# Optimization experiments

Measured on AMD Instinct MI355X. Metric: run time of the kernel, lower is better.

## Reference

```python
import jax, jax.numpy as jnp
import numpy as np

N_VARS, N_FACT, N_EDGES, D = 100000, 50000, 1000000, 128


def setup_inputs() -> dict:
    key = jax.random.key(0)
    ks = jax.random.split(key, 8)
    variables = jax.random.normal(ks[0], (N_VARS, D), dtype=jnp.float32)
    factors = jax.random.normal(ks[1], (N_FACT, D), dtype=jnp.float32)
    v_to_f = jax.random.randint(ks[2], (N_EDGES,), 0, N_VARS, dtype=jnp.int32)
    f_to_v = jax.random.randint(ks[3], (N_EDGES,), 0, N_FACT, dtype=jnp.int32)
    edge_attr = jax.random.normal(ks[4], (N_EDGES,), dtype=jnp.float32)
    # small init scale to keep activations sane
    W_msg = jax.random.normal(ks[5], (2 * D + 1, D), dtype=jnp.float32) * 0.05
    b_msg = jnp.zeros((D,), dtype=jnp.float32)
    W_comb = jax.random.normal(ks[6], (2 * D, D), dtype=jnp.float32) * 0.05
    b_comb = jnp.zeros((D,), dtype=jnp.float32)
    return dict(variables=variables, factors=factors, v_to_f=v_to_f,
                f_to_v=f_to_v, edge_attr=edge_attr, W_msg=W_msg, b_msg=b_msg,
                W_comb=W_comb, b_comb=b_comb)


def reference(variables, factors, v_to_f, f_to_v, edge_attr, W_msg, b_msg, W_comb, b_comb):
    # gather endpoint features per edge
    x_i = variables[v_to_f]                      # [E, D]
    x_j = factors[f_to_v]                        # [E, D]
    ea = jnp.zeros_like(edge_attr)[:, None]      # forward passes zeros_like(edge_attr)
    # per-edge message MLP (Linear + activation)
    m = jax.nn.relu(jnp.concatenate([x_i, x_j, ea], axis=-1) @ W_msg + b_msg)  # [E, D]
    # scatter-aggregate messages onto the variable (sender) nodes
    aggr_m = jax.ops.segment_sum(m, v_to_f, num_segments=variables.shape[0])   # [N_v, D]
    # concat + combine MLP + residual
    h = jax.nn.relu(jnp.concatenate([variables, aggr_m], axis=-1) @ W_comb + b_comb)
    return variables + h
```

## Files before the change

### kernel.cpp

```cpp
#include <hip/hip_runtime.h>

#define NV 100000
#define NF 50000
#define NE 1000000
#define NBV2 782
#define NBF2 391
#define NBH2 489

typedef unsigned short ushort_t;
typedef unsigned int uint_t;
typedef __attribute__((ext_vector_type(8))) short bf16x8;
typedef __attribute__((ext_vector_type(8))) _Float16 f16x8;
typedef __attribute__((ext_vector_type(2))) _Float16 f16x2;
typedef __attribute__((ext_vector_type(4))) float f32x4;
typedef __attribute__((ext_vector_type(4))) uint_t u32x4;


__device__ inline ushort_t f2bf(float x) {
    union { float f; uint_t u; } c; c.f = x;
    uint_t r = c.u + 0x7fffu + ((c.u >> 16) & 1u);
    return (ushort_t)(r >> 16);
}

__device__ inline uint_t packh2(float a, float b) {
    auto h = __builtin_amdgcn_cvt_pkrtz(a, b);
    return __builtin_bit_cast(uint_t, h);
}

__device__ inline bf16x8 cvt_frag(float4 lo, float4 hi) {
    uint_t a, b, c, d;
    asm("v_cvt_pk_bf16_f32 %0, %1, %2" : "=v"(a) : "v"(lo.x), "v"(lo.y));
    asm("v_cvt_pk_bf16_f32 %0, %1, %2" : "=v"(b) : "v"(lo.z), "v"(lo.w));
    asm("v_cvt_pk_bf16_f32 %0, %1, %2" : "=v"(c) : "v"(hi.x), "v"(hi.y));
    asm("v_cvt_pk_bf16_f32 %0, %1, %2" : "=v"(d) : "v"(hi.z), "v"(hi.w));
    u32x4 q = {a, b, c, d};
    return __builtin_bit_cast(bf16x8, q);
}

__device__ inline void gload_lds16(const void* g, void* l) {
    __builtin_amdgcn_global_load_lds(
        (const __attribute__((address_space(1))) void*)g,
        (__attribute__((address_space(3))) void*)l, 16, 0, 0);
}

__global__ __launch_bounds__(256) void scan_reduce(const int* __restrict__ deg, int* __restrict__ bsum) {
    __shared__ int s[256];
    int t = threadIdx.x, b = blockIdx.x;
    int base = b * 1024 + t * 4;
    int acc = 0;
#pragma unroll
    for (int j = 0; j < 4; j++) { int i = base + j; if (i < NV) acc += deg[i]; }
    s[t] = acc; __syncthreads();
    for (int off = 128; off > 0; off >>= 1) {
        if (t < off) s[t] += s[t + off];
        __syncthreads();
    }
    if (t == 0) bsum[b] = s[0];
}

__global__ __launch_bounds__(128) void scan_mid(int* __restrict__ bsum, int* __restrict__ offs, int nblk) {
    __shared__ int s[128];
    int t = threadIdx.x;
    int val = (t < nblk) ? bsum[t] : 0;
    s[t] = val; __syncthreads();
    for (int off = 1; off < 128; off <<= 1) {
        int x = (t >= off) ? s[t - off] : 0;
        __syncthreads();
        s[t] += x;
        __syncthreads();
    }
    if (t < nblk) bsum[t] = s[t] - val;
    if (t == 0) offs[NV] = NE;
}

__global__ __launch_bounds__(256) void scan_final(int* __restrict__ deg, const int* __restrict__ bsum,
                                                  int* __restrict__ offs) {
    __shared__ int s[256];
    int t = threadIdx.x, b = blockIdx.x;
    int base = b * 1024 + t * 4;
    int v[4];
#pragma unroll
    for (int j = 0; j < 4; j++) { int i = base + j; v[j] = (i < NV) ? deg[i] : 0; }
    int l = v[0] + v[1] + v[2] + v[3];
    s[t] = l; __syncthreads();
    for (int off = 1; off < 256; off <<= 1) {
        int x = (t >= off) ? s[t - off] : 0;
        __syncthreads();
        s[t] += x;
        __syncthreads();
    }
    int run = bsum[b] + s[t] - l;
#pragma unroll
    for (int j = 0; j < 4; j++) {
        int i = base + j;
        if (i < NV) { offs[i] = run; deg[i] = run; }
        run += v[j];
    }
}

__global__ __launch_bounds__(256) void scatter_k(const int* __restrict__ vtf, const int* __restrict__ ftv,
                                                 int* __restrict__ cursor, ushort_t* __restrict__ sf) {
    int e2 = blockIdx.x * 256 + threadIdx.x;
    if (e2 < NE / 2) {
        int2 v = *(const int2*)(vtf + e2 * 2);
        int2 f = *(const int2*)(ftv + e2 * 2);
        int p0 = atomicAdd(&cursor[v.x], 1);
        sf[p0] = (ushort_t)f.x;
        int p1 = atomicAdd(&cursor[v.y], 1);
        sf[p1] = (ushort_t)f.y;
    }
}

__global__ __launch_bounds__(256) void prep_w(const float* __restrict__ Wm, const float* __restrict__ Wc,
                                              ushort_t* __restrict__ frag) {
    int t = blockIdx.x * 256 + threadIdx.x;
    int mat = t >> 14;
    int idx = t & 16383;
    int k = idx >> 7, n = idx & 127;
    int srck = k;
    if (mat == 3) {
        int j = k >> 1;
        srck = (j & 15) + 32 * (j >> 4) + 16 * (k & 1);
    }
    const float* src = (mat < 2) ? (Wm + (size_t)mat * 16384) : (Wc + (size_t)(mat - 2) * 16384);
    float v = src[(size_t)srck * 128 + n];
    ushort_t outv;
    if (mat == 3) {
        _Float16 h = (_Float16)v;
        outv = __builtin_bit_cast(ushort_t, h);
    } else {
        outv = f2bf(v);
    }
    int kc = k >> 5, kk = k & 31, quad = kk >> 3, j = kk & 7;
    int ct = n >> 4, np = n & 15, lane = np + 16 * quad;
    frag[(size_t)mat * 16384 + (size_t)((kc * 8 + ct) * 64 + lane) * 8 + j] = outv;
}

__global__ __launch_bounds__(512, 4) void gemm_msg(const float* __restrict__ V,
                                                   const float* __restrict__ F,
                                                   const ushort_t* __restrict__ wfm,
                                                   const float* __restrict__ bias,
                                                   uint_t* __restrict__ u,
                                                   uint_t* __restrict__ w,
                                                   const int* __restrict__ vtf,
                                                   int* __restrict__ deg) {
    if (blockIdx.x < NBH2) {
        int e4 = blockIdx.x * 512 + threadIdx.x;
        if (e4 < NE / 4) {
            int4 vv = *(const int4*)(vtf + (size_t)e4 * 4);
            atomicAdd(&deg[vv.x], 1);
            atomicAdd(&deg[vv.y], 1);
            atomicAdd(&deg[vv.z], 1);
            atomicAdd(&deg[vv.w], 1);
        }
        return;
    }
    __shared__ ushort_t Bs[16384];

    const int bid = blockIdx.x - NBH2;
    const float* A; const ushort_t* wf; uint_t* C; const float* bs; int M, r0;
    if (bid < NBV2) { A = V; wf = wfm;         C = u; bs = bias;    M = NV; r0 = bid * 128; }
    else            { A = F; wf = wfm + 16384; C = w; bs = nullptr; M = NF; r0 = (bid - NBV2) * 128; }

    const int wv = threadIdx.x >> 6;
    const int lane = threadIdx.x & 63;
    const int quad = lane >> 4, np = lane & 15;
    const int arow = r0 + wv * 16 + np;
    const int ar = (arow < M) ? arow : (M - 1);

    {
        const char* gsrc = (const char*)wf;
        char* lbase = (char*)Bs;
#pragma unroll
        for (int i = 0; i < 4; i++) {
            int off = (wv * 4 + i) * 1024;
            gload_lds16(gsrc + off + lane * 16, lbase + off);
        }
    }
    const float* ap = A + (size_t)ar * 128 + quad * 8;
    float4 vlo[4], vhi[4];
#pragma unroll
    for (int kc = 0; kc < 4; kc++) {
        vlo[kc] = *(const float4*)(ap + kc * 32);
        vhi[kc] = *(const float4*)(ap + kc * 32 + 4);
    }
    float bb0[4], bb1[4];
#pragma unroll
    for (int g = 0; g < 4; g++) {
        bb0[g] = bs ? bs[np + 32 * g] : 0.f;
        bb1[g] = bs ? bs[np + 32 * g + 16] : 0.f;
    }

    __builtin_amdgcn_sched_barrier(0);
    asm volatile("s_waitcnt vmcnt(0)");
    __syncthreads();

    bf16x8 a[4];
#pragma unroll
    for (int kc = 0; kc < 4; kc++) a[kc] = cvt_frag(vlo[kc], vhi[kc]);

    f32x4 acc[8];
#pragma unroll
    for (int ct = 0; ct < 8; ct++) acc[ct] = (f32x4){0.f, 0.f, 0.f, 0.f};

#pragma unroll
    for (int kc = 0; kc < 4; kc++) {
        const ushort_t* wp = Bs + (size_t)(kc * 8 * 64 + lane) * 8;
#pragma unroll
        for (int ct = 0; ct < 8; ct++) {
            bf16x8 b = *(const bf16x8*)(wp + ct * 512);
            acc[ct] = __builtin_amdgcn_mfma_f32_16x16x32_bf16(a[kc], b, acc[ct], 0, 0, 0);
        }
    }

#pragma unroll
    for (int g = 0; g < 4; g++) {
#pragma unroll
        for (int r = 0; r < 4; r++) {
            int orow = r0 + wv * 16 + quad * 4 + r;
            if (orow < M)
                C[(size_t)orow * 64 + g * 16 + np] = packh2(acc[2 * g][r] + bb0[g],
                                                            acc[2 * g + 1][r] + bb1[g]);
        }
    }
}

__global__ __launch_bounds__(256, 6) void aggregate(const uint_t* __restrict__ u32,
                                                    const uint_t* __restrict__ w32,
                                                    const int* __restrict__ offs,
                                                    const ushort_t* __restrict__ sf,
                                                    uint_t* __restrict__ aggr32) {
    int v = (blockIdx.x * 256 + threadIdx.x) >> 6;
    int lane = threadIdx.x & 63;
    if (v >= NV) return;
    int i0 = offs[v], i1 = offs[v + 1];
    f16x2 uh = __builtin_bit_cast(f16x2, u32[(size_t)v * 64 + lane]);
    const f16x2 z2 = __builtin_bit_cast(f16x2, 0u);
    f16x2 acc[8];
#pragma unroll
    for (int j = 0; j < 8; j++) acc[j] = z2;
    for (int i = i0; i < i1; i += 8) {
        int f[8];
#pragma unroll
        for (int j = 0; j < 8; j++) {
            int idx = i + j; if (idx > i1 - 1) idx = i1 - 1;
            f[j] = sf[idx];
        }
        uint_t p[8];
#pragma unroll
        for (int j = 0; j < 8; j++) p[j] = w32[(size_t)f[j] * 64 + lane];
#pragma unroll
        for (int j = 0; j < 8; j++) {
            uint_t pj = (i + j < i1) ? p[j] : 0xFC00FC00u;
            f16x2 s = uh + __builtin_bit_cast(f16x2, pj);
            f16x2 r;
            asm("v_pk_max_f16 %0, %1, %2" : "=v"(r) : "v"(s), "v"(z2));
            acc[j] += r;
        }
    }
    f16x2 t0 = (acc[0] + acc[1]) + (acc[2] + acc[3]);
    f16x2 t1 = (acc[4] + acc[5]) + (acc[6] + acc[7]);
    f16x2 tt = t0 + t1;
    aggr32[(size_t)v * 64 + lane] = __builtin_bit_cast(uint_t, tt);
}

__global__ __launch_bounds__(512, 4) void gemm_final(const float* __restrict__ V,
                                                     const ushort_t* __restrict__ aggr,
                                                     const ushort_t* __restrict__ wfc,
                                                     const float* __restrict__ bias,
                                                     float* __restrict__ OUT, int M) {
    __shared__ ushort_t Bs[32768];

    const int wv = threadIdx.x >> 6;
    const int lane = threadIdx.x & 63;
    const int quad = lane >> 4, np = lane & 15;
    const int r0 = blockIdx.x * 128;
    const int arow = r0 + wv * 16 + np;
    const int ar = (arow < M) ? arow : (M - 1);

    {
        const char* gsrc = (const char*)wfc;
        char* lbase = (char*)Bs;
#pragma unroll
        for (int i = 0; i < 8; i++) {
            int off = (wv * 8 + i) * 1024;
            gload_lds16(gsrc + off + lane * 16, lbase + off);
        }
    }
    const float* ap = V + (size_t)ar * 128 + quad * 8;
    float4 vlo[4], vhi[4];
#pragma unroll
    for (int kc = 0; kc < 4; kc++) {
        vlo[kc] = *(const float4*)(ap + kc * 32);
        vhi[kc] = *(const float4*)(ap + kc * 32 + 4);
    }
    const ushort_t* agp = aggr + (size_t)ar * 128 + quad * 8;
    f16x8 af[4];
#pragma unroll
    for (int kc = 0; kc < 4; kc++) af[kc] = *(const f16x8*)(agp + kc * 32);
    float bb[8];
#pragma unroll
    for (int ct = 0; ct < 8; ct++) bb[ct] = bias[ct * 16 + np];

    __builtin_amdgcn_sched_barrier(0);
    asm volatile("s_waitcnt vmcnt(0)");
    __syncthreads();

    bf16x8 abf[4];
#pragma unroll
    for (int kc = 0; kc < 4; kc++) abf[kc] = cvt_frag(vlo[kc], vhi[kc]);

    f32x4 acc[8];
#pragma unroll
    for (int ct = 0; ct < 8; ct++) acc[ct] = (f32x4){0.f, 0.f, 0.f, 0.f};

#pragma unroll
    for (int kc = 0; kc < 4; kc++) {
        const ushort_t* wp = Bs + (size_t)(kc * 8 * 64 + lane) * 8;
#pragma unroll
        for (int ct = 0; ct < 8; ct++) {
            bf16x8 b = *(const bf16x8*)(wp + ct * 512);
            acc[ct] = __builtin_amdgcn_mfma_f32_16x16x32_bf16(abf[kc], b, acc[ct], 0, 0, 0);
        }
    }
#pragma unroll
    for (int kc = 0; kc < 4; kc++) {
        const ushort_t* wp = Bs + 16384 + (size_t)(kc * 8 * 64 + lane) * 8;
#pragma unroll
        for (int ct = 0; ct < 8; ct++) {
            f16x8 b = *(const f16x8*)(wp + ct * 512);
            acc[ct] = __builtin_amdgcn_mfma_f32_16x16x32_f16(af[kc], b, acc[ct], 0, 0, 0);
        }
    }

    const int orow0 = r0 + wv * 16 + quad * 4;
    float resid[32];
#pragma unroll
    for (int ct = 0; ct < 8; ct++)
#pragma unroll
        for (int r = 0; r < 4; r++) {
            int orow = orow0 + r;
            resid[ct * 4 + r] = (orow < M) ? V[(size_t)orow * 128 + ct * 16 + np] : 0.f;
        }
#pragma unroll
    for (int ct = 0; ct < 8; ct++)
#pragma unroll
        for (int r = 0; r < 4; r++) {
            int orow = orow0 + r;
            if (orow < M)
                OUT[(size_t)orow * 128 + ct * 16 + np] =
                    resid[ct * 4 + r] + fmaxf(acc[ct][r] + bb[ct], 0.f);
        }
}

extern "C" void kernel_launch(void* const* d_in, const int* in_sizes, int n_in,
                              void* d_out, int out_size, void* d_ws, size_t ws_size,
                              hipStream_t stream) {
    const float* variables = (const float*)d_in[0];
    const float* factors   = (const float*)d_in[1];
    const int*   v_to_f    = (const int*)d_in[2];
    const int*   f_to_v    = (const int*)d_in[3];
    const float* W_msg     = (const float*)d_in[5];
    const float* b_msg     = (const float*)d_in[6];
    const float* W_comb    = (const float*)d_in[7];
    const float* b_comb    = (const float*)d_in[8];
    float* out = (float*)d_out;

    ushort_t* wfrag = (ushort_t*)d_ws;
    uint_t*   u     = (uint_t*)(wfrag + 4 * 16384);
    uint_t*   w     = u + (size_t)NV * 64;
    uint_t*   aggr  = w + (size_t)NF * 64;
    ushort_t* sf    = (ushort_t*)(aggr + (size_t)NV * 64);
    int*      deg   = (int*)(sf + NE);
    int*      offs  = deg + NV;
    int*      bsum  = offs + NV + 1;

    const int NBLK = (NV + 1023) / 1024;

    prep_w<<<256, 256, 0, stream>>>(W_msg, W_comb, wfrag);

    hipMemsetAsync(deg, 0, (size_t)NV * sizeof(int), stream);

    gemm_msg<<<NBH2 + NBV2 + NBF2, 512, 0, stream>>>(variables, factors, wfrag, b_msg,
                                                     u, w, v_to_f, deg);

    scan_reduce<<<NBLK, 256, 0, stream>>>(deg, bsum);
    scan_mid<<<1, 128, 0, stream>>>(bsum, offs, NBLK);
    scan_final<<<NBLK, 256, 0, stream>>>(deg, bsum, offs);
    scatter_k<<<(NE / 2 + 255) / 256, 256, 0, stream>>>(v_to_f, f_to_v, deg, sf);

    aggregate<<<(NV * 64) / 256, 256, 0, stream>>>(u, w, offs, sf, aggr);

    gemm_final<<<NBV2, 512, 0, stream>>>(variables, (const ushort_t*)aggr, wfrag + 2 * 16384,
                                         b_comb, out, NV);
}
```

Measured before the change: 317.7 us.

## Process multiple row tiles per GEMM block with prefetch and split histogram kernel

Both GEMM kernels now cover 256 rows per block, looping over sub-tiles. Each block loads the weight fragment into LDS once and reuses it, and prefetches the next tile's activations into registers while the current tile's MFMAs run. gemm_msg drops to 256 threads per block. The degree histogram moves from extra blocks of gemm_msg into its own kernel launch. This amortizes the weight staging per block and hides the global load latency, at the cost of fewer blocks (less parallelism) and an extra launch.

```diff
diff --git a/kernel.cpp b/kernel.cpp
--- a/kernel.cpp
+++ b/kernel.cpp
@@ -3,9 +3,9 @@
 #define NV 100000
 #define NF 50000
 #define NE 1000000
-#define NBV2 782
-#define NBF2 391
-#define NBH2 489
+#define GMV 391
+#define GMF 196
+#define GFN 391
 
 typedef unsigned short ushort_t;
 typedef unsigned int uint_t;
@@ -41,6 +41,17 @@
     __builtin_amdgcn_global_load_lds(
         (const __attribute__((address_space(1))) void*)g,
         (__attribute__((address_space(3))) void*)l, 16, 0, 0);
+}
+
+__global__ __launch_bounds__(256) void hist_k(const int* __restrict__ vtf, int* __restrict__ deg) {
+    int e4 = blockIdx.x * 256 + threadIdx.x;
+    if (e4 < NE / 4) {
+        int4 v = *(const int4*)(vtf + (size_t)e4 * 4);
+        atomicAdd(&deg[v.x], 1);
+        atomicAdd(&deg[v.y], 1);
+        atomicAdd(&deg[v.z], 1);
+        atomicAdd(&deg[v.w], 1);
+    }
 }
 
 __global__ __launch_bounds__(256) void scan_reduce(const int* __restrict__ deg, int* __restrict__ bsum) {
@@ -136,53 +147,39 @@
     frag[(size_t)mat * 16384 + (size_t)((kc * 8 + ct) * 64 + lane) * 8 + j] = outv;
 }
 
-__global__ __launch_bounds__(512, 4) void gemm_msg(const float* __restrict__ V,
+__global__ __launch_bounds__(256, 4) void gemm_msg(const float* __restrict__ V,
                                                    const float* __restrict__ F,
                                                    const ushort_t* __restrict__ wfm,
                                                    const float* __restrict__ bias,
                                                    uint_t* __restrict__ u,
-                                                   uint_t* __restrict__ w,
-                                                   const int* __restrict__ vtf,
-                                                   int* __restrict__ deg) {
-    if (blockIdx.x < NBH2) {
-        int e4 = blockIdx.x * 512 + threadIdx.x;
-        if (e4 < NE / 4) {
-            int4 vv = *(const int4*)(vtf + (size_t)e4 * 4);
-            atomicAdd(&deg[vv.x], 1);
-            atomicAdd(&deg[vv.y], 1);
-            atomicAdd(&deg[vv.z], 1);
-            atomicAdd(&deg[vv.w], 1);
-        }
-        return;
-    }
+                                                   uint_t* __restrict__ w) {
     __shared__ ushort_t Bs[16384];
 
-    const int bid = blockIdx.x - NBH2;
     const float* A; const ushort_t* wf; uint_t* C; const float* bs; int M, r0;
-    if (bid < NBV2) { A = V; wf = wfm;         C = u; bs = bias;    M = NV; r0 = bid * 128; }
-    else            { A = F; wf = wfm + 16384; C = w; bs = nullptr; M = NF; r0 = (bid - NBV2) * 128; }
+    if (blockIdx.x < GMV) { A = V; wf = wfm;         C = u; bs = bias;    M = NV; r0 = blockIdx.x * 256; }
+    else                  { A = F; wf = wfm + 16384; C = w; bs = nullptr; M = NF; r0 = (blockIdx.x - GMV) * 256; }
 
     const int wv = threadIdx.x >> 6;
     const int lane = threadIdx.x & 63;
     const int quad = lane >> 4, np = lane & 15;
-    const int arow = r0 + wv * 16 + np;
-    const int ar = (arow < M) ? arow : (M - 1);
 
     {
         const char* gsrc = (const char*)wf;
         char* lbase = (char*)Bs;
-#pragma unroll
-        for (int i = 0; i < 4; i++) {
-            int off = (wv * 4 + i) * 1024;
-            gload_lds16(gsrc + off + lane * 16, lbase + off);
-        }
-    }
-    const float* ap = A + (size_t)ar * 128 + quad * 8;
+        int toff = threadIdx.x * 16;
+#pragma unroll
+        for (int i = 0; i < 8; i++) gload_lds16(gsrc + i * 4096 + toff, lbase + i * 4096 + toff);
+    }
+
     float4 vlo[4], vhi[4];
-#pragma unroll
-    for (int kc = 0; kc < 4; kc++) {
-        vlo[kc] = *(const float4*)(ap + kc * 32);
-        vhi[kc] = *(const float4*)(ap + kc * 32 + 4);
+    {
+        int ar0 = r0 + wv * 16 + np; if (ar0 >= M) ar0 = M - 1;
+        const float* ap = A + (size_t)ar0 * 128 + quad * 8;
+#pragma unroll
+        for (int kc = 0; kc < 4; kc++) {
+            vlo[kc] = *(const float4*)(ap + kc * 32);
+            vhi[kc] = *(const float4*)(ap + kc * 32 + 4);
+        }
     }
     float bb0[4], bb1[4];
 #pragma unroll
@@ -191,36 +188,49 @@
         bb1[g] = bs ? bs[np + 32 * g + 16] : 0.f;
     }
 
+    asm volatile("s_waitcnt vmcnt(0)" ::: "memory");
     __builtin_amdgcn_sched_barrier(0);
-    asm volatile("s_waitcnt vmcnt(0)");
     __syncthreads();
 
-    bf16x8 a[4];
-#pragma unroll
-    for (int kc = 0; kc < 4; kc++) a[kc] = cvt_frag(vlo[kc], vhi[kc]);
-
-    f32x4 acc[8];
-#pragma unroll
-    for (int ct = 0; ct < 8; ct++) acc[ct] = (f32x4){0.f, 0.f, 0.f, 0.f};
-
-#pragma unroll
-    for (int kc = 0; kc < 4; kc++) {
-        const ushort_t* wp = Bs + (size_t)(kc * 8 * 64 + lane) * 8;
-#pragma unroll
-        for (int ct = 0; ct < 8; ct++) {
-            bf16x8 b = *(const bf16x8*)(wp + ct * 512);
-            acc[ct] = __builtin_amdgcn_mfma_f32_16x16x32_bf16(a[kc], b, acc[ct], 0, 0, 0);
-        }
-    }
-
-#pragma unroll
-    for (int g = 0; g < 4; g++) {
-#pragma unroll
-        for (int r = 0; r < 4; r++) {
-            int orow = r0 + wv * 16 + quad * 4 + r;
-            if (orow < M)
-                C[(size_t)orow * 64 + g * 16 + np] = packh2(acc[2 * g][r] + bb0[g],
-                                                            acc[2 * g + 1][r] + bb1[g]);
+#pragma unroll
+    for (int t = 0; t < 4; t++) {
+        bf16x8 a[4];
+#pragma unroll
+        for (int kc = 0; kc < 4; kc++) a[kc] = cvt_frag(vlo[kc], vhi[kc]);
+
+        if (t < 3) {
+            int nr = r0 + (t + 1) * 64 + wv * 16 + np; if (nr >= M) nr = M - 1;
+            const float* ap = A + (size_t)nr * 128 + quad * 8;
+#pragma unroll
+            for (int kc = 0; kc < 4; kc++) {
+                vlo[kc] = *(const float4*)(ap + kc * 32);
+                vhi[kc] = *(const float4*)(ap + kc * 32 + 4);
+            }
+        }
+        __builtin_amdgcn_sched_barrier(0);
+
+        f32x4 acc[8];
+#pragma unroll
+        for (int ct = 0; ct < 8; ct++) acc[ct] = (f32x4){0.f, 0.f, 0.f, 0.f};
+#pragma unroll
+        for (int kc = 0; kc < 4; kc++) {
+            const ushort_t* wp = Bs + (size_t)(kc * 8 * 64 + lane) * 8;
+#pragma unroll
+            for (int ct = 0; ct < 8; ct++) {
+                bf16x8 b = *(const bf16x8*)(wp + ct * 512);
+                acc[ct] = __builtin_amdgcn_mfma_f32_16x16x32_bf16(a[kc], b, acc[ct], 0, 0, 0);
+            }
+        }
+
+#pragma unroll
+        for (int g = 0; g < 4; g++) {
+#pragma unroll
+            for (int r = 0; r < 4; r++) {
+                int orow = r0 + t * 64 + wv * 16 + quad * 4 + r;
+                if (orow < M)
+                    C[(size_t)orow * 64 + g * 16 + np] = packh2(acc[2 * g][r] + bb0[g],
+                                                                acc[2 * g + 1][r] + bb1[g]);
+            }
         }
     }
 }
@@ -274,83 +284,104 @@
     const int wv = threadIdx.x >> 6;
     const int lane = threadIdx.x & 63;
     const int quad = lane >> 4, np = lane & 15;
-    const int r0 = blockIdx.x * 128;
-    const int arow = r0 + wv * 16 + np;
-    const int ar = (arow < M) ? arow : (M - 1);
+    const int r0 = blockIdx.x * 256;
 
     {
         const char* gsrc = (const char*)wfc;
         char* lbase = (char*)Bs;
-#pragma unroll
-        for (int i = 0; i < 8; i++) {
-            int off = (wv * 8 + i) * 1024;
-            gload_lds16(gsrc + off + lane * 16, lbase + off);
-        }
-    }
-    const float* ap = V + (size_t)ar * 128 + quad * 8;
+        int toff = threadIdx.x * 16;
+#pragma unroll
+        for (int i = 0; i < 8; i++) gload_lds16(gsrc + i * 8192 + toff, lbase + i * 8192 + toff);
+    }
+
     float4 vlo[4], vhi[4];
-#pragma unroll
-    for (int kc = 0; kc < 4; kc++) {
-        vlo[kc] = *(const float4*)(ap + kc * 32);
-        vhi[kc] = *(const float4*)(ap + kc * 32 + 4);
-    }
-    const ushort_t* agp = aggr + (size_t)ar * 128 + quad * 8;
     f16x8 af[4];
-#pragma unroll
-    for (int kc = 0; kc < 4; kc++) af[kc] = *(const f16x8*)(agp + kc * 32);
+    {
+        int ar0 = r0 + wv * 16 + np; if (ar0 >= M) ar0 = M - 1;
+        const float* ap = V + (size_t)ar0 * 128 + quad * 8;
+#pragma unroll
+        for (int kc = 0; kc < 4; kc++) {
+            vlo[kc] = *(const float4*)(ap + kc * 32);
+            vhi[kc] = *(const float4*)(ap + kc * 32 + 4);
+        }
+        const ushort_t* agp = aggr + (size_t)ar0 * 128 + quad * 8;
+#pragma unroll
+        for (int kc = 0; kc < 4; kc++) af[kc] = *(const f16x8*)(agp + kc * 32);
+    }
     float bb[8];
 #pragma unroll
     for (int ct = 0; ct < 8; ct++) bb[ct] = bias[ct * 16 + np];
 
+    asm volatile("s_waitcnt vmcnt(0)" ::: "memory");
     __builtin_amdgcn_sched_barrier(0);
-    asm volatile("s_waitcnt vmcnt(0)");
     __syncthreads();
 
-    bf16x8 abf[4];
-#pragma unroll
-    for (int kc = 0; kc < 4; kc++) abf[kc] = cvt_frag(vlo[kc], vhi[kc]);
-
-    f32x4 acc[8];
-#pragma unroll
-    for (int ct = 0; ct < 8; ct++) acc[ct] = (f32x4){0.f, 0.f, 0.f, 0.f};
-
-#pragma unroll
-    for (int kc = 0; kc < 4; kc++) {
-        const ushort_t* wp = Bs + (size_t)(kc * 8 * 64 + lane) * 8;
-#pragma unroll
-        for (int ct = 0; ct < 8; ct++) {
-            bf16x8 b = *(const bf16x8*)(wp + ct * 512);
-            acc[ct] = __builtin_amdgcn_mfma_f32_16x16x32_bf16(abf[kc], b, acc[ct], 0, 0, 0);
-        }
-    }
-#pragma unroll
-    for (int kc = 0; kc < 4; kc++) {
-        const ushort_t* wp = Bs + 16384 + (size_t)(kc * 8 * 64 + lane) * 8;
-#pragma unroll
-        for (int ct = 0; ct < 8; ct++) {
-            f16x8 b = *(const f16x8*)(wp + ct * 512);
-            acc[ct] = __builtin_amdgcn_mfma_f32_16x16x32_f16(af[kc], b, acc[ct], 0, 0, 0);
-        }
-    }
-
-    const int orow0 = r0 + wv * 16 + quad * 4;
-    float resid[32];
-#pragma unroll
-    for (int ct = 0; ct < 8; ct++)
-#pragma unroll
-        for (int r = 0; r < 4; r++) {
-            int orow = orow0 + r;
-            resid[ct * 4 + r] = (orow < M) ? V[(size_t)orow * 128 + ct * 16 + np] : 0.f;
-        }
-#pragma unroll
-    for (int ct = 0; ct < 8; ct++)
-#pragma unroll
-        for (int r = 0; r < 4; r++) {
-            int orow = orow0 + r;
-            if (orow < M)
-                OUT[(size_t)orow * 128 + ct * 16 + np] =
-                    resid[ct * 4 + r] + fmaxf(acc[ct][r] + bb[ct], 0.f);
-        }
+#pragma unroll
+    for (int t = 0; t < 2; t++) {
+        bf16x8 abf[4];
+#pragma unroll
+        for (int kc = 0; kc < 4; kc++) abf[kc] = cvt_frag(vlo[kc], vhi[kc]);
+
+        if (t < 1) {
+            int nr = r0 + 128 + wv * 16 + np; if (nr >= M) nr = M - 1;
+            const float* ap = V + (size_t)nr * 128 + quad * 8;
+#pragma unroll
+            for (int kc = 0; kc < 4; kc++) {
+                vlo[kc] = *(const float4*)(ap + kc * 32);
+                vhi[kc] = *(const float4*)(ap + kc * 32 + 4);
+            }
+        }
+        __builtin_amdgcn_sched_barrier(0);
+
+        f32x4 acc[8];
+#pragma unroll
+        for (int ct = 0; ct < 8; ct++) acc[ct] = (f32x4){0.f, 0.f, 0.f, 0.f};
+
+#pragma unroll
+        for (int kc = 0; kc < 4; kc++) {
+            const ushort_t* wp = Bs + (size_t)(kc * 8 * 64 + lane) * 8;
+#pragma unroll
+            for (int ct = 0; ct < 8; ct++) {
+                bf16x8 b = *(const bf16x8*)(wp + ct * 512);
+                acc[ct] = __builtin_amdgcn_mfma_f32_16x16x32_bf16(abf[kc], b, acc[ct], 0, 0, 0);
+            }
+        }
+#pragma unroll
+        for (int kc = 0; kc < 4; kc++) {
+            const ushort_t* wp = Bs + 16384 + (size_t)(kc * 8 * 64 + lane) * 8;
+#pragma unroll
+            for (int ct = 0; ct < 8; ct++) {
+                f16x8 b = *(const f16x8*)(wp + ct * 512);
+                acc[ct] = __builtin_amdgcn_mfma_f32_16x16x32_f16(af[kc], b, acc[ct], 0, 0, 0);
+            }
+        }
+        if (t < 1) {
+            int nr = r0 + 128 + wv * 16 + np; if (nr >= M) nr = M - 1;
+            const ushort_t* agp = aggr + (size_t)nr * 128 + quad * 8;
+#pragma unroll
+            for (int kc = 0; kc < 4; kc++) af[kc] = *(const f16x8*)(agp + kc * 32);
+        }
+        __builtin_amdgcn_sched_barrier(0);
+
+        const int orow0 = r0 + t * 128 + wv * 16 + quad * 4;
+        float resid[32];
+#pragma unroll
+        for (int ct = 0; ct < 8; ct++)
+#pragma unroll
+            for (int r = 0; r < 4; r++) {
+                int orow = orow0 + r;
+                resid[ct * 4 + r] = (orow < M) ? V[(size_t)orow * 128 + ct * 16 + np] : 0.f;
+            }
+#pragma unroll
+        for (int ct = 0; ct < 8; ct++)
+#pragma unroll
+            for (int r = 0; r < 4; r++) {
+                int orow = orow0 + r;
+                if (orow < M)
+                    OUT[(size_t)orow * 128 + ct * 16 + np] =
+                        resid[ct * 4 + r] + fmaxf(acc[ct][r] + bb[ct], 0.f);
+            }
+    }
 }
 
 extern "C" void kernel_launch(void* const* d_in, const int* in_sizes, int n_in,
@@ -380,9 +411,9 @@
     prep_w<<<256, 256, 0, stream>>>(W_msg, W_comb, wfrag);
 
     hipMemsetAsync(deg, 0, (size_t)NV * sizeof(int), stream);
-
-    gemm_msg<<<NBH2 + NBV2 + NBF2, 512, 0, stream>>>(variables, factors, wfrag, b_msg,
-                                                     u, w, v_to_f, deg);
+    hist_k<<<(NE / 4 + 255) / 256, 256, 0, stream>>>(v_to_f, deg);
+
+    gemm_msg<<<GMV + GMF, 256, 0, stream>>>(variables, factors, wfrag, b_msg, u, w);
 
     scan_reduce<<<NBLK, 256, 0, stream>>>(deg, bsum);
     scan_mid<<<1, 128, 0, stream>>>(bsum, offs, NBLK);
@@ -391,6 +422,6 @@
 
     aggregate<<<(NV * 64) / 256, 256, 0, stream>>>(u, w, offs, sf, aggr);
 
-    gemm_final<<<NBV2, 512, 0, stream>>>(variables, (const ushort_t*)aggr, wfrag + 2 * 16384,
-                                         b_comb, out, NV);
-}
+    gemm_final<<<GFN, 512, 0, stream>>>(variables, (const ushort_t*)aggr, wfrag + 2 * 16384,
+                                        b_comb, out, NV);
+}
```

Result: slower. 325.8 us (+2.6%).
